# Optimization experiments

Measured on AMD Instinct MI355X. Metric: run time of the kernel, lower is better.

The kernel has to match this reference:

```python
import jax, jax.numpy as jnp
import numpy as np

N_NODES = 50000
N_EDGES = 800000
D_IN = 256
D_H = 128
D_OUT = 2
NUM_FC = 2


def setup_inputs() -> dict:
    key = jax.random.key(0)
    ks = jax.random.split(key, 12)
    s = 0.05
    inp = {
        "x": jax.random.normal(ks[0], (N_NODES, D_IN), dtype=jnp.float32),
        "edge_index": jax.random.randint(ks[1], (2, N_EDGES), 0, N_NODES, dtype=jnp.int64),
        "W_gcn": jax.random.normal(ks[2], (D_IN, D_H), dtype=jnp.float32) * s,
        "b_gcn": jnp.zeros((D_H,), dtype=jnp.float32),
        "fc1_W": jax.random.normal(ks[3], (D_H, D_H), dtype=jnp.float32) * s,
        "fc1_b": jnp.zeros((D_H,), dtype=jnp.float32),
        "fc2_W": jax.random.normal(ks[4], (D_H, D_H), dtype=jnp.float32) * s,
        "fc2_b": jnp.zeros((D_H,), dtype=jnp.float32),
        "out_W": jax.random.normal(ks[5], (D_H, D_OUT), dtype=jnp.float32) * s,
        "out_b": jnp.zeros((D_OUT,), dtype=jnp.float32),
    }
    return inp


def _gcn_conv(x, edge_index, W, b):
    # PyG GCNConv: add self-loops, symmetric normalization D^-1/2 (A+I) D^-1/2, then aggregate X@W.
    n = x.shape[0]
    loops = jnp.arange(n, dtype=edge_index.dtype)
    src = jnp.concatenate([edge_index[0], loops])
    dst = jnp.concatenate([edge_index[1], loops])
    h = x @ W  # [N, D_H]
    deg = jax.ops.segment_sum(jnp.ones_like(dst, dtype=h.dtype), dst, num_segments=n)
    dinv = jnp.where(deg > 0, jax.lax.rsqrt(deg), 0.0)
    norm = dinv[src] * dinv[dst]  # [E+N]
    msg = h[src] * norm[:, None]
    out = jax.ops.segment_sum(msg, dst, num_segments=n)
    return out + b


def _mlp_stack(h, fc1_W, fc1_b, fc2_W, fc2_b):
    # fc -> relu (dropout is eval-mode identity)
    h = jax.nn.relu(h @ fc1_W + fc1_b)
    h = jax.nn.relu(h @ fc2_W + fc2_b)
    return h


def reference(x, edge_index, W_gcn, b_gcn, fc1_W, fc1_b, fc2_W, fc2_b, out_W, out_b):
    h = jax.nn.relu(_gcn_conv(x, edge_index, W_gcn, b_gcn))  # [N, D_H]
    h = _mlp_stack(h, fc1_W, fc1_b, fc2_W, fc2_b)
    # edge-pair gather + average
    edge_x = (h[edge_index[0]] + h[edge_index[1]]) * 0.5  # [E, D_H]
    # note: same fc weights reused, faithful to source
    edge_x = _mlp_stack(edge_x, fc1_W, fc1_b, fc2_W, fc2_b)
    scores = edge_x @ out_W + out_b  # [E, D_OUT]
    return jax.nn.log_softmax(scores, axis=1)
```

## Files before the change

kernel.cpp:

```cpp
#include <hip/hip_runtime.h>

#define NN 50000
#define NE 800000
#define DIN 256
#define DH 128
#define BCAP 64

#define GEMM_BLKS 391
#define SWZ_BLKS 32
#define FILL_BLKS (NE / 256)

typedef float f32x4 __attribute__((ext_vector_type(4)));
typedef __bf16 bf16x8 __attribute__((ext_vector_type(8)));
typedef unsigned short u16;
typedef unsigned int u32;

__device__ __forceinline__ u16 f2b(float f) { return __builtin_bit_cast(u16, (__bf16)f); }
__device__ __forceinline__ float lo_f(u32 u) { return (float)__builtin_bit_cast(__bf16, (u16)(u & 0xFFFFu)); }
__device__ __forceinline__ float hi_f(u32 u) { return (float)__builtin_bit_cast(__bf16, (u16)(u >> 16)); }

__device__ __forceinline__ f32x4 mfma16(bf16x8 a, bf16x8 b, f32x4 c) {
    return __builtin_amdgcn_mfma_f32_16x16x32_bf16(a, b, c, 0, 0, 0);
}

__global__ __launch_bounds__(256) void k_prep_gemm(const float* __restrict__ x,
                                                   const float* __restrict__ w1,
                                                   const float* __restrict__ w2,
                                                   const float* __restrict__ wg,
                                                   u16* __restrict__ w12f, u16* __restrict__ wgf,
                                                   const int* __restrict__ ei,
                                                   int* __restrict__ cnt, int* __restrict__ bucket,
                                                   u16* __restrict__ h0pre) {
    int b = blockIdx.x;
    if (b < GEMM_BLKS) {
        int wave = threadIdx.x >> 6, lane = threadIdx.x & 63;
        int l15 = lane & 15, q = lane >> 4;
        int rowBase = b * 128 + wave * 32;

        bf16x8 a[2][8];
#pragma unroll
        for (int mi = 0; mi < 2; ++mi) {
            int r = rowBase + mi * 16 + l15; if (r >= NN) r = NN - 1;
            const float* rp = x + (size_t)r * DIN + q * 8;
#pragma unroll
            for (int kt = 0; kt < 8; ++kt) {
                f32x4 f0 = *(const f32x4*)(rp + kt * 32);
                f32x4 f1 = *(const f32x4*)(rp + kt * 32 + 4);
                bf16x8 aa;
#pragma unroll
                for (int j = 0; j < 4; ++j) { aa[j] = (__bf16)f0[j]; aa[j + 4] = (__bf16)f1[j]; }
                a[mi][kt] = aa;
            }
        }
        f32x4 z = {0.f, 0.f, 0.f, 0.f};
        f32x4 acc[2][8];
#pragma unroll
        for (int mi = 0; mi < 2; ++mi)
#pragma unroll
            for (int nt = 0; nt < 8; ++nt) acc[mi][nt] = z;
#pragma unroll
        for (int kt = 0; kt < 8; ++kt)
#pragma unroll
            for (int nt = 0; nt < 8; ++nt) {
                bf16x8 bb = *(const bf16x8*)(wgf + ((kt * 8 + nt) * 64 + lane) * 8);
                acc[0][nt] = mfma16(a[0][kt], bb, acc[0][nt]);
                acc[1][nt] = mfma16(a[1][kt], bb, acc[1][nt]);
            }
#pragma unroll
        for (int mi = 0; mi < 2; ++mi)
#pragma unroll
            for (int rg = 0; rg < 4; ++rg) {
                int r = rowBase + mi * 16 + q * 4 + rg;
                if (r < NN) {
#pragma unroll
                    for (int nt = 0; nt < 8; ++nt)
                        h0pre[r * DH + nt * 16 + l15] = f2b(acc[mi][nt][rg]);
                }
            }
    } else if (b < GEMM_BLKS + SWZ_BLKS) {
        int t = (b - GEMM_BLKS) * 256 + threadIdx.x;
        const float* src; u16* dst; int id;
        if (t < 2048)      { src = w1; dst = w12f;          id = t; }
        else if (t < 4096) { src = w2; dst = w12f + 16384;  id = t - 2048; }
        else               { src = wg; dst = wgf;           id = t - 4096; }
        int lane = id & 63, frag = id >> 6;
        int kt = frag >> 3, nt = frag & 7;
        int k0 = kt * 32 + (lane >> 4) * 8, n = nt * 16 + (lane & 15);
        u16 v[8];
#pragma unroll
        for (int j = 0; j < 8; ++j) v[j] = f2b(src[(k0 + j) * 128 + n]);
#pragma unroll
        for (int j = 0; j < 8; ++j) dst[id * 8 + j] = v[j];
    } else {
        int e = (b - GEMM_BLKS - SWZ_BLKS) * 256 + threadIdx.x;
        int d = ei[NE + e];
        int pos = atomicAdd(&cnt[d], 1);
        bucket[d * BCAP + pos] = ei[e];
    }
}

__global__ __launch_bounds__(256) void k_agg_mlp(const u16* __restrict__ h0pre,
                                                 const int* __restrict__ cnt,
                                                 const int* __restrict__ bucket,
                                                 const float* __restrict__ bg,
                                                 const u16* __restrict__ wf,
                                                 const float* __restrict__ b1,
                                                 const float* __restrict__ b2,
                                                 u16* __restrict__ gh) {
    __shared__ __align__(16) u16 wlds[16384];
    __shared__ __align__(16) u16 sct[4][2176];
    {
        const uint4* s = (const uint4*)wf;
        uint4* d = (uint4*)wlds;
        for (int i = threadIdx.x; i < 2048; i += 256) d[i] = s[i];
    }
    __syncthreads();

    int wave = threadIdx.x >> 6, lane = threadIdx.x & 63;
    int qw = lane >> 4, l16 = lane & 15;
    const uint4* h4p = (const uint4*)h0pre;
    u16* sw = sct[wave];

#pragma unroll 1
    for (int p = 0; p < 4; ++p) {
        int vl = p * 4 + qw;
        int v = blockIdx.x * 64 + wave * 16 + vl;
        if (v >= NN) v = NN - 1;

        int deg = cnt[v];
        float dv = rsqrtf((float)deg + 1.0f);
        uint4 su = h4p[v * 16 + l16];
        float acc0[8], acc1[8];
#pragma unroll
        for (int i = 0; i < 8; ++i) acc1[i] = 0.f;
        acc0[0] = lo_f(su.x) * dv; acc0[1] = hi_f(su.x) * dv;
        acc0[2] = lo_f(su.y) * dv; acc0[3] = hi_f(su.y) * dv;
        acc0[4] = lo_f(su.z) * dv; acc0[5] = hi_f(su.z) * dv;
        acc0[6] = lo_f(su.w) * dv; acc0[7] = hi_f(su.w) * dv;

        const int* bk = bucket + v * BCAP;
        int j = 0;
        for (; j + 8 <= deg; j += 8) {
            int idx[8]; uint4 u[8]; float ds[8];
#pragma unroll
            for (int k = 0; k < 8; ++k) idx[k] = bk[j + k];
#pragma unroll
            for (int k = 0; k < 8; ++k) u[k] = h4p[idx[k] * 16 + l16];
#pragma unroll
            for (int k = 0; k < 8; ++k) ds[k] = rsqrtf((float)cnt[idx[k]] + 1.0f);
#pragma unroll
            for (int k = 0; k < 8; ++k) {
                float* A = (k & 1) ? acc1 : acc0;
                A[0] = fmaf(lo_f(u[k].x), ds[k], A[0]);
                A[1] = fmaf(hi_f(u[k].x), ds[k], A[1]);
                A[2] = fmaf(lo_f(u[k].y), ds[k], A[2]);
                A[3] = fmaf(hi_f(u[k].y), ds[k], A[3]);
                A[4] = fmaf(lo_f(u[k].z), ds[k], A[4]);
                A[5] = fmaf(hi_f(u[k].z), ds[k], A[5]);
                A[6] = fmaf(lo_f(u[k].w), ds[k], A[6]);
                A[7] = fmaf(hi_f(u[k].w), ds[k], A[7]);
            }
        }
        for (; j + 2 <= deg; j += 2) {
            int ia = bk[j], ib = bk[j + 1];
            uint4 ua = h4p[ia * 16 + l16];
            uint4 ub = h4p[ib * 16 + l16];
            float da = rsqrtf((float)cnt[ia] + 1.0f);
            float db = rsqrtf((float)cnt[ib] + 1.0f);
            acc0[0] = fmaf(lo_f(ua.x), da, acc0[0]); acc0[1] = fmaf(hi_f(ua.x), da, acc0[1]);
            acc0[2] = fmaf(lo_f(ua.y), da, acc0[2]); acc0[3] = fmaf(hi_f(ua.y), da, acc0[3]);
            acc0[4] = fmaf(lo_f(ua.z), da, acc0[4]); acc0[5] = fmaf(hi_f(ua.z), da, acc0[5]);
            acc0[6] = fmaf(lo_f(ua.w), da, acc0[6]); acc0[7] = fmaf(hi_f(ua.w), da, acc0[7]);
            acc1[0] = fmaf(lo_f(ub.x), db, acc1[0]); acc1[1] = fmaf(hi_f(ub.x), db, acc1[1]);
            acc1[2] = fmaf(lo_f(ub.y), db, acc1[2]); acc1[3] = fmaf(hi_f(ub.y), db, acc1[3]);
            acc1[4] = fmaf(lo_f(ub.z), db, acc1[4]); acc1[5] = fmaf(hi_f(ub.z), db, acc1[5]);
            acc1[6] = fmaf(lo_f(ub.w), db, acc1[6]); acc1[7] = fmaf(hi_f(ub.w), db, acc1[7]);
        }
        for (; j < deg; ++j) {
            int ia = bk[j];
            uint4 u = h4p[ia * 16 + l16];
            float da = rsqrtf((float)cnt[ia] + 1.0f);
            acc0[0] = fmaf(lo_f(u.x), da, acc0[0]); acc0[1] = fmaf(hi_f(u.x), da, acc0[1]);
            acc0[2] = fmaf(lo_f(u.y), da, acc0[2]); acc0[3] = fmaf(hi_f(u.y), da, acc0[3]);
            acc0[4] = fmaf(lo_f(u.z), da, acc0[4]); acc0[5] = fmaf(hi_f(u.z), da, acc0[5]);
            acc0[6] = fmaf(lo_f(u.w), da, acc0[6]); acc0[7] = fmaf(hi_f(u.w), da, acc0[7]);
        }
        float4 bg0 = ((const float4*)bg)[l16 * 2];
        float4 bg1 = ((const float4*)bg)[l16 * 2 + 1];
        float r[8];
#pragma unroll
        for (int i = 0; i < 8; ++i) r[i] = acc0[i] + acc1[i];
        r[0] = fmaxf(r[0] * dv + bg0.x, 0.f); r[1] = fmaxf(r[1] * dv + bg0.y, 0.f);
        r[2] = fmaxf(r[2] * dv + bg0.z, 0.f); r[3] = fmaxf(r[3] * dv + bg0.w, 0.f);
        r[4] = fmaxf(r[4] * dv + bg1.x, 0.f); r[5] = fmaxf(r[5] * dv + bg1.y, 0.f);
        r[6] = fmaxf(r[6] * dv + bg1.z, 0.f); r[7] = fmaxf(r[7] * dv + bg1.w, 0.f);
        uint4 outw;
        outw.x = (u32)f2b(r[0]) | ((u32)f2b(r[1]) << 16);
        outw.y = (u32)f2b(r[2]) | ((u32)f2b(r[3]) << 16);
        outw.z = (u32)f2b(r[4]) | ((u32)f2b(r[5]) << 16);
        outw.w = (u32)f2b(r[6]) | ((u32)f2b(r[7]) << 16);
        *(uint4*)(sw + vl * 136 + l16 * 8) = outw;
    }

    int l15 = lane & 15, q = lane >> 4;
    int rowBase = blockIdx.x * 64 + wave * 16;
    float bb1[8], bb2[8];
#pragma unroll
    for (int nt = 0; nt < 8; ++nt) { bb1[nt] = b1[nt * 16 + l15]; bb2[nt] = b2[nt * 16 + l15]; }

    bf16x8 a[4];
#pragma unroll
    for (int kt = 0; kt < 4; ++kt) a[kt] = *(const bf16x8*)(sw + l15 * 136 + kt * 32 + q * 8);
    f32x4 z = {0.f, 0.f, 0.f, 0.f};
    f32x4 acc1[8];
#pragma unroll
    for (int nt = 0; nt < 8; ++nt) acc1[nt] = z;
#pragma unroll
    for (int kt = 0; kt < 4; ++kt)
#pragma unroll
        for (int nt = 0; nt < 8; ++nt) {
            bf16x8 b = *(const bf16x8*)(wlds + (kt * 8 + nt) * 512 + lane * 8);
            acc1[nt] = mfma16(a[kt], b, acc1[nt]);
        }

    bf16x8 a2[4];
#pragma unroll
    for (int nt = 0; nt < 8; ++nt)
#pragma unroll
        for (int rg = 0; rg < 4; ++rg) {
            float v = acc1[nt][rg] + bb1[nt];
            v = v > 0.f ? v : 0.f;
            sw[(q * 4 + rg) * 136 + nt * 16 + l15] = f2b(v);
        }
#pragma unroll
    for (int kt = 0; kt < 4; ++kt)
        a2[kt] = *(const bf16x8*)(sw + l15 * 136 + kt * 32 + q * 8);
    __syncthreads();
    {
        const uint4* s = (const uint4*)(wf + 16384);
        uint4* d = (uint4*)wlds;
        for (int i = threadIdx.x; i < 2048; i += 256) d[i] = s[i];
    }
    __syncthreads();
    f32x4 acc2[8];
#pragma unroll
    for (int nt = 0; nt < 8; ++nt) acc2[nt] = z;
#pragma unroll
    for (int kt = 0; kt < 4; ++kt)
#pragma unroll
        for (int nt = 0; nt < 8; ++nt) {
            bf16x8 b = *(const bf16x8*)(wlds + (kt * 8 + nt) * 512 + lane * 8);
            acc2[nt] = mfma16(a2[kt], b, acc2[nt]);
        }
    bf16x8 a3[4];
#pragma unroll
    for (int nt = 0; nt < 8; ++nt)
#pragma unroll
        for (int rg = 0; rg < 4; ++rg) {
            float v = acc2[nt][rg] + bb2[nt];
            v = v > 0.f ? v : 0.f;
            sw[(q * 4 + rg) * 136 + nt * 16 + l15] = f2b(v);
        }
#pragma unroll
    for (int kt = 0; kt < 4; ++kt)
        a3[kt] = *(const bf16x8*)(sw + l15 * 136 + kt * 32 + q * 8);
    __syncthreads();
    {
        const uint4* s = (const uint4*)wf;
        uint4* d = (uint4*)wlds;
        for (int i = threadIdx.x; i < 2048; i += 256) d[i] = s[i];
    }
    __syncthreads();
    f32x4 acc3[8];
#pragma unroll
    for (int nt = 0; nt < 8; ++nt) acc3[nt] = z;
#pragma unroll
    for (int kt = 0; kt < 4; ++kt)
#pragma unroll
        for (int nt = 0; nt < 8; ++nt) {
            bf16x8 b = *(const bf16x8*)(wlds + (kt * 8 + nt) * 512 + lane * 8);
            acc3[nt] = mfma16(a3[kt], b, acc3[nt]);
        }
#pragma unroll
    for (int nt = 0; nt < 8; ++nt)
#pragma unroll
        for (int rg = 0; rg < 4; ++rg) {
            int r = rowBase + q * 4 + rg;
            if (r < NN)
                gh[r * DH + nt * 16 + l15] = f2b(0.5f * acc3[nt][rg] + 0.5f * bb1[nt]);
        }
}

__global__ __launch_bounds__(256, 3) void k_edge_mlp(const u16* __restrict__ gh,
                                                     const int* __restrict__ ei,
                                                     const u16* __restrict__ wf,
                                                     const float* __restrict__ b2,
                                                     const float* __restrict__ ow,
                                                     const float* __restrict__ ob,
                                                     float2* __restrict__ outp) {
    __shared__ __align__(16) u16 wlds[16384];
    {
        const uint4* s = (const uint4*)(wf + 16384);
        uint4* d = (uint4*)wlds;
        for (int i = threadIdx.x; i < 2048; i += 256) d[i] = s[i];
    }
    int wave = threadIdx.x >> 6, lane = threadIdx.x & 63;
    int l15 = lane & 15, q = lane >> 4;
    int eBase = blockIdx.x * 256 + wave * 64;

    int se[4], de[4];
#pragma unroll
    for (int ti = 0; ti < 4; ++ti) {
        int e = eBase + ti * 16 + l15;
        se[ti] = ei[e];
        de[ti] = ei[NE + e];
    }
    bf16x8 gsA[4], gdA[4], gsB[4], gdB[4];
    {
        const u16* ps = gh + se[0] * DH + q * 8;
        const u16* pd = gh + de[0] * DH + q * 8;
#pragma unroll
        for (int kt = 0; kt < 4; ++kt) {
            gsA[kt] = *(const bf16x8*)(ps + kt * 32);
            gdA[kt] = *(const bf16x8*)(pd + kt * 32);
        }
    }
    {
        const u16* ps = gh + se[1] * DH + q * 8;
        const u16* pd = gh + de[1] * DH + q * 8;
#pragma unroll
        for (int kt = 0; kt < 4; ++kt) {
            gsB[kt] = *(const bf16x8*)(ps + kt * 32);
            gdB[kt] = *(const bf16x8*)(pd + kt * 32);
        }
    }
    float bb2[8], owp0[8], owp1[8];
#pragma unroll
    for (int nt = 0; nt < 8; ++nt) {
        int k = nt * 16 + l15;
        bb2[nt] = b2[k];
        owp0[nt] = ow[2 * k];
        owp1[nt] = ow[2 * k + 1];
    }
    float ob0 = ob[0], ob1 = ob[1];
    __syncthreads();
    f32x4 z = {0.f, 0.f, 0.f, 0.f};

#pragma unroll
    for (int ti = 0; ti < 4; ++ti) {
        bf16x8 fs[4], fd[4];
#pragma unroll
        for (int kt = 0; kt < 4; ++kt) {
            fs[kt] = (ti & 1) ? gsB[kt] : gsA[kt];
            fd[kt] = (ti & 1) ? gdB[kt] : gdA[kt];
        }
        if (ti + 2 < 4) {
            const u16* ps = gh + se[ti + 2] * DH + q * 8;
            const u16* pd = gh + de[ti + 2] * DH + q * 8;
#pragma unroll
            for (int kt = 0; kt < 4; ++kt) {
                if (ti & 1) { gsB[kt] = *(const bf16x8*)(ps + kt * 32); gdB[kt] = *(const bf16x8*)(pd + kt * 32); }
                else        { gsA[kt] = *(const bf16x8*)(ps + kt * 32); gdA[kt] = *(const bf16x8*)(pd + kt * 32); }
            }
        }
        bf16x8 a2[4];
#pragma unroll
        for (int kt = 0; kt < 4; ++kt) {
            bf16x8 r;
#pragma unroll
            for (int j = 0; j < 8; ++j) {
                float t = (float)fs[kt][j] + (float)fd[kt][j];
                r[j] = (__bf16)(t > 0.f ? t : 0.f);
            }
            a2[kt] = r;
        }
        f32x4 acc2[8];
#pragma unroll
        for (int nt = 0; nt < 8; ++nt) acc2[nt] = z;
#pragma unroll
        for (int kt = 0; kt < 4; ++kt)
#pragma unroll
            for (int nt = 0; nt < 8; ++nt) {
                bf16x8 b = *(const bf16x8*)(wlds + (kt * 8 + nt) * 512 + lane * 8);
                acc2[nt] = mfma16(a2[kt], b, acc2[nt]);
            }
#pragma unroll
        for (int rg = 0; rg < 4; ++rg) {
            float p0 = 0.f, p1 = 0.f;
#pragma unroll
            for (int nt = 0; nt < 8; ++nt) {
                float t = acc2[nt][rg] + bb2[nt];
                t = t > 0.f ? t : 0.f;
                p0 += t * owp0[nt];
                p1 += t * owp1[nt];
            }
#pragma unroll
            for (int m = 1; m < 16; m <<= 1) {
                p0 += __shfl_xor(p0, m, 64);
                p1 += __shfl_xor(p1, m, 64);
            }
            if (l15 == 0) {
                int e = eBase + ti * 16 + q * 4 + rg;
                float s0 = p0 + ob0, s1 = p1 + ob1;
                float mx = fmaxf(s0, s1);
                float lse = mx + __logf(__expf(s0 - mx) + __expf(s1 - mx));
                outp[e] = make_float2(s0 - lse, s1 - lse);
            }
        }
    }
}

extern "C" void kernel_launch(void* const* d_in, const int* in_sizes, int n_in,
                              void* d_out, int out_size, void* d_ws, size_t ws_size,
                              hipStream_t stream) {
    const float* x  = (const float*)d_in[0];
    const int* ei   = (const int*)d_in[1];
    const float* wg = (const float*)d_in[2];
    const float* bg = (const float*)d_in[3];
    const float* w1 = (const float*)d_in[4];
    const float* b1 = (const float*)d_in[5];
    const float* w2 = (const float*)d_in[6];
    const float* b2 = (const float*)d_in[7];
    const float* ow = (const float*)d_in[8];
    const float* ob = (const float*)d_in[9];
    float2* out = (float2*)d_out;

    char* ws = (char*)d_ws;
    size_t off = 0;
    auto alloc = [&](size_t bytes) { void* p = ws + off; off += (bytes + 255) & ~(size_t)255; return p; };
    u16* h0      = (u16*)alloc((size_t)NN * DH * 2);
    u16* ghb     = (u16*)alloc((size_t)NN * DH * 2);
    int* bucket  = (int*)alloc((size_t)NN * BCAP * 4);
    int* cnt     = (int*)alloc((size_t)NN * 4);
    u16* w12f    = (u16*)alloc(65536);
    u16* wgf     = (u16*)alloc(65536);

    hipMemsetAsync(cnt, 0, (size_t)NN * 4, stream);
    k_prep_gemm<<<GEMM_BLKS + SWZ_BLKS + FILL_BLKS, 256, 0, stream>>>(
        x, w1, w2, wg, w12f, wgf, ei, cnt, bucket, h0);
    k_agg_mlp<<<(NN + 63) / 64, 256, 0, stream>>>(h0, cnt, bucket, bg, w12f, b1, b2, ghb);
    k_edge_mlp<<<NE / 256, 256, 0, stream>>>(ghb, ei, w12f, b2, ow, ob, out);
}
```

Measured before the change: 284.4 us.

## Read MLP weights from global instead of LDS and shrink edge prefetch depth

The node aggregation+MLP kernel no longer stages the fc1/fc2 weights into LDS with block-wide barriers. Each MFMA B-fragment is now loaded straight from global memory, relying on cache hits, which removes 32KB of LDS per block and the syncthreads between layers. The edge MLP kernel cuts gather prefetch from two tiles to one and raises its launch-bounds occupancy target from 3 to 4 blocks. In exchange it takes more cache traffic for the weights and may hide less gather latency.

```diff
diff --git a/kernel.cpp b/kernel.cpp
--- a/kernel.cpp
+++ b/kernel.cpp
@@ -107,24 +107,17 @@
                                                  const float* __restrict__ b1,
                                                  const float* __restrict__ b2,
                                                  u16* __restrict__ gh) {
-    __shared__ __align__(16) u16 wlds[16384];
     __shared__ __align__(16) u16 sct[4][2176];
-    {
-        const uint4* s = (const uint4*)wf;
-        uint4* d = (uint4*)wlds;
-        for (int i = threadIdx.x; i < 2048; i += 256) d[i] = s[i];
-    }
-    __syncthreads();
-
     int wave = threadIdx.x >> 6, lane = threadIdx.x & 63;
     int qw = lane >> 4, l16 = lane & 15;
     const uint4* h4p = (const uint4*)h0pre;
     u16* sw = sct[wave];
+    int rowBase = blockIdx.x * 64 + wave * 16;
 
 #pragma unroll 1
     for (int p = 0; p < 4; ++p) {
         int vl = p * 4 + qw;
-        int v = blockIdx.x * 64 + wave * 16 + vl;
+        int v = rowBase + vl;
         if (v >= NN) v = NN - 1;
 
         int deg = cnt[v];
@@ -203,7 +196,6 @@
     }
 
     int l15 = lane & 15, q = lane >> 4;
-    int rowBase = blockIdx.x * 64 + wave * 16;
     float bb1[8], bb2[8];
 #pragma unroll
     for (int nt = 0; nt < 8; ++nt) { bb1[nt] = b1[nt * 16 + l15]; bb2[nt] = b2[nt * 16 + l15]; }
@@ -219,7 +211,7 @@
     for (int kt = 0; kt < 4; ++kt)
 #pragma unroll
         for (int nt = 0; nt < 8; ++nt) {
-            bf16x8 b = *(const bf16x8*)(wlds + (kt * 8 + nt) * 512 + lane * 8);
+            bf16x8 b = *(const bf16x8*)(wf + (kt * 8 + nt) * 512 + lane * 8);
             acc1[nt] = mfma16(a[kt], b, acc1[nt]);
         }
 
@@ -235,13 +227,7 @@
 #pragma unroll
     for (int kt = 0; kt < 4; ++kt)
         a2[kt] = *(const bf16x8*)(sw + l15 * 136 + kt * 32 + q * 8);
-    __syncthreads();
-    {
-        const uint4* s = (const uint4*)(wf + 16384);
-        uint4* d = (uint4*)wlds;
-        for (int i = threadIdx.x; i < 2048; i += 256) d[i] = s[i];
-    }
-    __syncthreads();
+
     f32x4 acc2[8];
 #pragma unroll
     for (int nt = 0; nt < 8; ++nt) acc2[nt] = z;
@@ -249,7 +235,7 @@
     for (int kt = 0; kt < 4; ++kt)
 #pragma unroll
         for (int nt = 0; nt < 8; ++nt) {
-            bf16x8 b = *(const bf16x8*)(wlds + (kt * 8 + nt) * 512 + lane * 8);
+            bf16x8 b = *(const bf16x8*)(wf + 16384 + (kt * 8 + nt) * 512 + lane * 8);
             acc2[nt] = mfma16(a2[kt], b, acc2[nt]);
         }
     bf16x8 a3[4];
@@ -264,13 +250,7 @@
 #pragma unroll
     for (int kt = 0; kt < 4; ++kt)
         a3[kt] = *(const bf16x8*)(sw + l15 * 136 + kt * 32 + q * 8);
-    __syncthreads();
-    {
-        const uint4* s = (const uint4*)wf;
-        uint4* d = (uint4*)wlds;
-        for (int i = threadIdx.x; i < 2048; i += 256) d[i] = s[i];
-    }
-    __syncthreads();
+
     f32x4 acc3[8];
 #pragma unroll
     for (int nt = 0; nt < 8; ++nt) acc3[nt] = z;
@@ -278,7 +258,7 @@
     for (int kt = 0; kt < 4; ++kt)
 #pragma unroll
         for (int nt = 0; nt < 8; ++nt) {
-            bf16x8 b = *(const bf16x8*)(wlds + (kt * 8 + nt) * 512 + lane * 8);
+            bf16x8 b = *(const bf16x8*)(wf + (kt * 8 + nt) * 512 + lane * 8);
             acc3[nt] = mfma16(a3[kt], b, acc3[nt]);
         }
 #pragma unroll
@@ -291,7 +271,7 @@
         }
 }
 
-__global__ __launch_bounds__(256, 3) void k_edge_mlp(const u16* __restrict__ gh,
+__global__ __launch_bounds__(256, 4) void k_edge_mlp(const u16* __restrict__ gh,
                                                      const int* __restrict__ ei,
                                                      const u16* __restrict__ wf,
                                                      const float* __restrict__ b2,
@@ -315,23 +295,14 @@
         se[ti] = ei[e];
         de[ti] = ei[NE + e];
     }
-    bf16x8 gsA[4], gdA[4], gsB[4], gdB[4];
+    bf16x8 bs[4], bd[4];
     {
         const u16* ps = gh + se[0] * DH + q * 8;
         const u16* pd = gh + de[0] * DH + q * 8;
 #pragma unroll
         for (int kt = 0; kt < 4; ++kt) {
-            gsA[kt] = *(const bf16x8*)(ps + kt * 32);
-            gdA[kt] = *(const bf16x8*)(pd + kt * 32);
-        }
-    }
-    {
-        const u16* ps = gh + se[1] * DH + q * 8;
-        const u16* pd = gh + de[1] * DH + q * 8;
-#pragma unroll
-        for (int kt = 0; kt < 4; ++kt) {
-            gsB[kt] = *(const bf16x8*)(ps + kt * 32);
-            gdB[kt] = *(const bf16x8*)(pd + kt * 32);
+            bs[kt] = *(const bf16x8*)(ps + kt * 32);
+            bd[kt] = *(const bf16x8*)(pd + kt * 32);
         }
     }
     float bb2[8], owp0[8], owp1[8];
@@ -348,31 +319,25 @@
 
 #pragma unroll
     for (int ti = 0; ti < 4; ++ti) {
-        bf16x8 fs[4], fd[4];
-#pragma unroll
-        for (int kt = 0; kt < 4; ++kt) {
-            fs[kt] = (ti & 1) ? gsB[kt] : gsA[kt];
-            fd[kt] = (ti & 1) ? gdB[kt] : gdA[kt];
-        }
-        if (ti + 2 < 4) {
-            const u16* ps = gh + se[ti + 2] * DH + q * 8;
-            const u16* pd = gh + de[ti + 2] * DH + q * 8;
-#pragma unroll
-            for (int kt = 0; kt < 4; ++kt) {
-                if (ti & 1) { gsB[kt] = *(const bf16x8*)(ps + kt * 32); gdB[kt] = *(const bf16x8*)(pd + kt * 32); }
-                else        { gsA[kt] = *(const bf16x8*)(ps + kt * 32); gdA[kt] = *(const bf16x8*)(pd + kt * 32); }
-            }
-        }
         bf16x8 a2[4];
 #pragma unroll
         for (int kt = 0; kt < 4; ++kt) {
             bf16x8 r;
 #pragma unroll
             for (int j = 0; j < 8; ++j) {
-                float t = (float)fs[kt][j] + (float)fd[kt][j];
+                float t = (float)bs[kt][j] + (float)bd[kt][j];
                 r[j] = (__bf16)(t > 0.f ? t : 0.f);
             }
             a2[kt] = r;
+        }
+        if (ti + 1 < 4) {
+            const u16* ps = gh + se[ti + 1] * DH + q * 8;
+            const u16* pd = gh + de[ti + 1] * DH + q * 8;
+#pragma unroll
+            for (int kt = 0; kt < 4; ++kt) {
+                bs[kt] = *(const bf16x8*)(ps + kt * 32);
+                bd[kt] = *(const bf16x8*)(pd + kt * 32);
+            }
         }
         f32x4 acc2[8];
 #pragma unroll
```

Result: faster. 276.2 us (-2.9%).
